# Optimization experiments

Hardware: AMD Instinct MI355X
Metric: run time of the kernel (lower is better)

The kernel has to match this reference:

```python
import jax, jax.numpy as jnp
import numpy as np

B = 2048       # batch
N = 256        # num_memory_locations
M = 64         # memory_size
U = 512        # num_units
IN = 10        # num_bits_per_vector + 2
SHIFT = 1      # conv_shift_range
CLIP = 20.0


def setup_inputs() -> dict:
    key = jax.random.key(0)
    ks = jax.random.split(key, 20)
    s = 0.05
    A0 = jax.random.uniform(ks[5], (2, B, N), dtype=jnp.float32)
    A0 = A0 / jnp.sum(A0, axis=-1, keepdims=True)  # distribution-like prev attention
    return {
        'x_t':  jax.random.normal(ks[0], (B, IN), dtype=jnp.float32),
        'H0':   jax.random.normal(ks[1], (B, U), dtype=jnp.float32) * s,
        'C0':   jax.random.normal(ks[2], (B, U), dtype=jnp.float32) * s,
        'm0':   jax.random.normal(ks[3], (B, N, M), dtype=jnp.float32) * s,
        'R0':   jax.random.normal(ks[4], (B, M), dtype=jnp.float32) * s,
        'A0':   A0,
        'Wprep': jax.random.normal(ks[6], (M, U), dtype=jnp.float32) * s,
        'bprep': jnp.zeros((U,), dtype=jnp.float32),
        'Wx':   jax.random.normal(ks[7], (IN + U, 4 * U), dtype=jnp.float32) * s,
        'Wh':   jax.random.normal(ks[8], (U, 4 * U), dtype=jnp.float32) * s,
        'bl':   jnp.zeros((4 * U,), dtype=jnp.float32),
        'Wr':   jax.random.normal(ks[9], (U, M + 6), dtype=jnp.float32) * s,
        'br':   jnp.zeros((M + 6,), dtype=jnp.float32),
        'Ww':   jax.random.normal(ks[10], (U, 3 * M + 6), dtype=jnp.float32) * s,
        'bw':   jnp.zeros((3 * M + 6,), dtype=jnp.float32),
        'Wo':   jax.random.normal(ks[11], (U + M, U), dtype=jnp.float32) * s,
        'bo':   jnp.zeros((U,), dtype=jnp.float32),
    }


def _addressing(head, m_tm1, a_tm1):
    # head: (B, >=M+6); m_tm1: (B,N,M); a_tm1: (B,N)
    k = jnp.tanh(head[:, :M])                                   # (B,M)
    beta = jax.nn.softplus(head[:, M])                          # (B,)
    g = jax.nn.sigmoid(head[:, M + 1])                          # (B,)
    s = jax.nn.softmax(head[:, M + 2:M + 2 + 2 * SHIFT + 1], axis=-1)  # (B,3)
    gamma = jax.nn.softplus(head[:, M + 2 + 2 * SHIFT + 1])     # (B,)
    # cosine similarity content addressing
    ip = jnp.einsum('bnm,bm->bn', m_tm1, k)                     # (B,N)
    k_norm = jnp.sqrt(jnp.sum(k * k, axis=1, keepdims=True))    # (B,1)
    m_norm = jnp.sqrt(jnp.sum(m_tm1 * m_tm1, axis=2))           # (B,N)
    K = ip / (k_norm * m_norm + 1e-8)
    w_c = jax.nn.softmax(beta[:, None] * K, axis=1)             # exp/sum == softmax
    w_g = g[:, None] * w_c + (1.0 - g[:, None]) * a_tm1
    # circular convolution: s placed at offsets [0..SHIFT] and [-SHIFT..-1]
    s_full = jnp.concatenate(
        [s[:, :SHIFT + 1], jnp.zeros((s.shape[0], N - (2 * SHIFT + 1)), s.dtype), s[:, -SHIFT:]],
        axis=1)                                                 # (B,N)
    idx = (jnp.arange(N)[:, None] - jnp.arange(N)[None, :]) % N  # (N,N)
    w_conv = jnp.einsum('bij,bj->bi', s_full[:, idx], w_g)       # w[i]=sum_j w_g[j]*s[(i-j)%N]
    w_sharp = w_conv ** gamma[:, None]
    return w_sharp / jnp.sum(w_sharp, axis=1, keepdims=True)


def reference(x_t, H0, C0, m0, R0, A0, Wprep, bprep, Wx, Wh, bl, Wr, br, Ww, bw, Wo, bo):
    # prep from previous reads
    h = R0 @ Wprep + bprep                                      # (B,U)
    # single-layer LSTM controller
    z = jnp.concatenate([x_t, h], axis=1) @ Wx + H0 @ Wh + bl   # (B,4U)
    i, f, g_, o = jnp.split(z, 4, axis=1)
    c_t = jax.nn.sigmoid(f) * C0 + jax.nn.sigmoid(i) * jnp.tanh(g_)
    h = jax.nn.sigmoid(o) * jnp.tanh(c_t)
    h = jnp.clip(h, -CLIP, CLIP)
    # heads
    r_out = h @ Wr + br                                         # (B, M+6)
    w_out = h @ Ww + bw                                         # (B, 3M+6)
    w_read = _addressing(r_out, m0, A0[0])                      # (B,N)
    w_write = _addressing(w_out, m0, A0[1])                     # (B,N)
    # read from OLD memory (as in original)
    R_t = jnp.einsum('bn,bnm->bm', w_read, m0)                  # (B,M)
    # write: erase + add
    del_v = jax.nn.sigmoid(w_out[:, -2 * M:-M])                 # (B,M)
    add_v = jnp.tanh(w_out[:, -M:])                             # (B,M)
    ww = w_write[:, :, None]                                    # (B,N,1)
    m_t = m0 * (1.0 - ww * del_v[:, None, :]) + ww * add_v[:, None, :]
    y_t = jnp.clip(jnp.concatenate([h, R_t], axis=1) @ Wo + bo, -CLIP, CLIP)
    return (y_t, m_t, R_t, w_read, w_write)
```

## Files before the change

### kernel.cpp

```cpp
#include <hip/hip_runtime.h>


using u16   = unsigned short;
using bfrag = __attribute__((ext_vector_type(8))) short;
using f4    = __attribute__((ext_vector_type(4))) float;

__device__ __forceinline__ float bf2f(u16 s){ union{float f;unsigned u;}v; v.u=((unsigned)s)<<16; return v.f; }
__device__ __forceinline__ u16 f2bf(float f){ union{float f;unsigned u;}v; v.f=f; unsigned r=v.u+0x7fffu+((v.u>>16)&1u); return (u16)(r>>16); }
__device__ __forceinline__ void bfpair(unsigned pr, float&a, float&b){ union{float f;unsigned u;}x,y; x.u=pr<<16; y.u=pr&0xffff0000u; a=x.f; b=y.f; }
__device__ __forceinline__ unsigned packbf(float a, float b){ return (unsigned)f2bf(a) | ((unsigned)f2bf(b)<<16); }
__device__ __forceinline__ float sigm(float x){ return 1.f/(1.f+expf(-x)); }
__device__ __forceinline__ float softplus_(float x){ return fmaxf(x,0.f)+log1pf(expf(-fabsf(x))); }

__device__ __forceinline__ void gld16(const u16* g, u16* l){
    __builtin_amdgcn_global_load_lds((const __attribute__((address_space(1))) unsigned*)g,
                                     (__attribute__((address_space(3))) unsigned*)l, 16, 0, 0);
}


__global__ __launch_bounds__(256) void k_wt_lstm(const float* __restrict__ Wx, const float* __restrict__ Wh,
                                                 u16* __restrict__ Wt){
    __shared__ float t[32][33];
    int n0 = blockIdx.x*32, k0 = blockIdx.y*32;
    int tx = threadIdx.x & 31, ty = threadIdx.x >> 5;
    #pragma unroll
    for(int r=0;r<4;r++){
        int k = k0 + ty*4 + r, n = n0 + tx;
        float v;
        if(k < 522)       v = Wx[k*2048 + n];
        else if(k < 1034) v = Wh[(k-522)*2048 + n];
        else              v = 0.f;
        t[ty*4+r][tx] = v;
    }
    __syncthreads();
    #pragma unroll
    for(int r=0;r<4;r++){
        int n = n0 + ty*4 + r, k = k0 + tx;
        Wt[n*1056 + k] = f2bf(t[tx][ty*4+r]);
    }
}

__global__ __launch_bounds__(256) void k_wt_heads(const float* __restrict__ Wr, const float* __restrict__ Ww,
                                                  u16* __restrict__ Wt){
    __shared__ float t[32][33];
    int n0 = blockIdx.x*32, k0 = blockIdx.y*32;
    int tx = threadIdx.x & 31, ty = threadIdx.x >> 5;
    #pragma unroll
    for(int r=0;r<4;r++){
        int k = k0 + ty*4 + r, n = n0 + tx;
        float v;
        if(n < 70)        v = Wr[k*70 + n];
        else if(n < 268)  v = Ww[k*198 + (n-70)];
        else              v = 0.f;
        t[ty*4+r][tx] = v;
    }
    __syncthreads();
    #pragma unroll
    for(int r=0;r<4;r++){
        int n = n0 + ty*4 + r, k = k0 + tx;
        Wt[n*512 + k] = f2bf(t[tx][ty*4+r]);
    }
}

__global__ __launch_bounds__(256) void k_wt_out(const float* __restrict__ Wo, u16* __restrict__ Wt){
    __shared__ float t[32][33];
    int n0 = blockIdx.x*32, k0 = blockIdx.y*32;
    int tx = threadIdx.x & 31, ty = threadIdx.x >> 5;
    #pragma unroll
    for(int r=0;r<4;r++){
        int k = k0 + ty*4 + r, n = n0 + tx;
        t[ty*4+r][tx] = Wo[k*512 + n];
    }
    __syncthreads();
    #pragma unroll
    for(int r=0;r<4;r++){
        int n = n0 + ty*4 + r, k = k0 + tx;
        Wt[n*576 + k] = f2bf(t[tx][ty*4+r]);
    }
}

__global__ __launch_bounds__(256) void k_abuild(const float* __restrict__ x, const float* __restrict__ H0,
                                                const float* __restrict__ R0, const float* __restrict__ Wprep,
                                                const float* __restrict__ bprep, u16* __restrict__ A){
    int flat = blockIdx.x*256 + threadIdx.x;
    int b = flat >> 9, u = flat & 511;
    u16* Ab = A + (size_t)b*1056;
    float acc = bprep[u];
    const float* r = R0 + b*64;
    #pragma unroll 8
    for(int m=0;m<64;m++) acc += r[m] * Wprep[m*512+u];
    Ab[10+u] = f2bf(acc);
    Ab[522+u] = f2bf(H0[b*512+u]);
    if(u<10) Ab[u] = f2bf(x[b*10+u]);
    if(u<22) Ab[1034+u] = 0;
}

__device__ __forceinline__ void gemm128(const u16* __restrict__ A, int lda,
                                        const u16* __restrict__ Bt, int ldb,
                                        int bm, int bn, int kiters,
                                        u16* Al, u16* Bl, f4 acc[4][4]){
    int tid = threadIdx.x, w = tid>>6, lane = tid&63, quad = lane>>4, l16 = lane&15;
    int wr = w>>1, wc = w&1;
    f4 z4 = {0.f,0.f,0.f,0.f};
    #pragma unroll
    for(int i=0;i<4;i++)
        #pragma unroll
        for(int j=0;j<4;j++) acc[i][j] = z4;
    int rA0 = tid>>2, kc = tid&3;
    int rA1 = rA0 + 64;
    const u16* ga0 = A  + (size_t)(bm+rA0)*lda + kc*8;
    const u16* ga1 = A  + (size_t)(bm+rA1)*lda + kc*8;
    const u16* gb0 = Bt + (size_t)(bn+rA0)*ldb + kc*8;
    const u16* gb1 = Bt + (size_t)(bn+rA1)*ldb + kc*8;
    u16* lA0 = Al + (w*64)*8;
    u16* lA1 = Al + (256 + w*64)*8;
    u16* lB0 = Bl + (w*64)*8;
    u16* lB1 = Bl + (256 + w*64)*8;
    for(int kt=0; kt<kiters; kt++){
        __syncthreads();
        gld16(ga0, lA0); gld16(ga1, lA1);
        gld16(gb0, lB0); gld16(gb1, lB1);
        ga0 += 32; ga1 += 32; gb0 += 32; gb1 += 32;
        __syncthreads();
        bfrag af[4], bf[4];
        #pragma unroll
        for(int i=0;i<4;i++) af[i] = *(const bfrag*)&Al[(wr*64 + i*16 + l16)*32 + quad*8];
        #pragma unroll
        for(int j=0;j<4;j++) bf[j] = *(const bfrag*)&Bl[(wc*64 + j*16 + l16)*32 + quad*8];
        #pragma unroll
        for(int i=0;i<4;i++)
            #pragma unroll
            for(int j=0;j<4;j++)
                acc[i][j] = __builtin_amdgcn_mfma_f32_16x16x32_bf16(af[i], bf[j], acc[i][j], 0, 0, 0);
    }
}

__global__ __launch_bounds__(256) void k_gemm_lstm(const u16* __restrict__ A, const u16* __restrict__ Wt,
                                                   float* __restrict__ z){
    __shared__ u16 Al[128*32], Bl[128*32];
    f4 acc[4][4];
    int bm = blockIdx.x*128, bn = blockIdx.y*128;
    gemm128(A, 1056, Wt, 1056, bm, bn, 33, Al, Bl, acc);
    int lane = threadIdx.x&63, quad = lane>>4, l16 = lane&15, w = threadIdx.x>>6;
    int wr = w>>1, wc = w&1;
    #pragma unroll
    for(int i=0;i<4;i++){
        #pragma unroll
        for(int j=0;j<4;j++){
            int col = bn + wc*64 + j*16 + l16;
            #pragma unroll
            for(int r=0;r<4;r++){
                int row = bm + wr*64 + i*16 + quad*4 + r;
                z[(size_t)row*2048 + col] = acc[i][j][r];
            }
        }
    }
}

__global__ __launch_bounds__(256) void k_gates(const float* __restrict__ z, const float* __restrict__ C0,
                                               const float* __restrict__ bl, u16* __restrict__ A2){
    int flat = blockIdx.x*256 + threadIdx.x;
    int b = flat>>9, u = flat&511;
    const float* zb = z + (size_t)b*2048;
    float zi = zb[u]      + bl[u];
    float zf = zb[512+u]  + bl[512+u];
    float zg = zb[1024+u] + bl[1024+u];
    float zo = zb[1536+u] + bl[1536+u];
    float c  = sigm(zf)*C0[b*512+u] + sigm(zi)*tanhf(zg);
    float hv = sigm(zo)*tanhf(c);
    hv = fminf(fmaxf(hv,-20.f),20.f);
    A2[(size_t)b*576 + u] = f2bf(hv);
}

__global__ __launch_bounds__(256) void k_gemm_heads(const u16* __restrict__ A2, const u16* __restrict__ Wt,
                                                    const float* __restrict__ br, const float* __restrict__ bw,
                                                    float* __restrict__ rout, float* __restrict__ wout){
    __shared__ u16 Al[128*32], Bl[128*32];
    f4 acc[4][4];
    int bm = blockIdx.x*128, bn = blockIdx.y*128;
    gemm128(A2, 576, Wt, 512, bm, bn, 16, Al, Bl, acc);
    int lane = threadIdx.x&63, quad = lane>>4, l16 = lane&15, w = threadIdx.x>>6;
    int wr = w>>1, wc = w&1;
    #pragma unroll
    for(int i=0;i<4;i++){
        #pragma unroll
        for(int j=0;j<4;j++){
            int col = bn + wc*64 + j*16 + l16;
            if(col >= 268) continue;
            #pragma unroll
            for(int r=0;r<4;r++){
                int row = bm + wr*64 + i*16 + quad*4 + r;
                float v = acc[i][j][r];
                if(col < 70) rout[(size_t)row*70 + col]        = v + br[col];
                else         wout[(size_t)row*198 + (col-70)]  = v + bw[col-70];
            }
        }
    }
}

__global__ __launch_bounds__(256) void k_gemm_out(const u16* __restrict__ A2, const u16* __restrict__ Wt,
                                                  const float* __restrict__ bo, float* __restrict__ y){
    __shared__ u16 Al[128*32], Bl[128*32];
    f4 acc[4][4];
    int bm = blockIdx.x*128, bn = blockIdx.y*128;
    gemm128(A2, 576, Wt, 576, bm, bn, 18, Al, Bl, acc);
    int lane = threadIdx.x&63, quad = lane>>4, l16 = lane&15, w = threadIdx.x>>6;
    int wr = w>>1, wc = w&1;
    #pragma unroll
    for(int i=0;i<4;i++){
        #pragma unroll
        for(int j=0;j<4;j++){
            int col = bn + wc*64 + j*16 + l16;
            float bias = bo[col];
            #pragma unroll
            for(int r=0;r<4;r++){
                int row = bm + wr*64 + i*16 + quad*4 + r;
                float v = acc[i][j][r] + bias;
                v = fminf(fmaxf(v,-20.f),20.f);
                y[(size_t)row*512 + col] = v;
            }
        }
    }
}

__global__ __launch_bounds__(256, 6) void k_addr(const float* __restrict__ m0, const float* __restrict__ A0,
                                              const float* __restrict__ rout, const float* __restrict__ wout,
                                              u16* __restrict__ A2,
                                              float* __restrict__ out_mt, float* __restrict__ out_rt,
                                              float* __restrict__ out_wr, float* __restrict__ out_ww){
    __shared__ __align__(16) float kk_s[2][64];
    __shared__ float knorm_s[2];
    __shared__ float sc[2][6];
    __shared__ float wgrr[512];
    __shared__ float wsel[2][256];
    __shared__ __align__(16) float dv[64], avv[64];
    __shared__ float wpart[4][6];
    int tid = threadIdx.x, b = blockIdx.x;
    int lane = tid & 63, w = tid >> 6;

    float a0r = A0[b*256 + tid];
    float a1r = A0[524288 + b*256 + tid];

    if(tid < 128){
        int hh = tid >> 6, m = lane;
        float kv = tanhf(hh ? wout[b*198 + m] : rout[b*70 + m]);
        kk_s[hh][m] = kv;
        float s2 = kv*kv;
        #pragma unroll
        for(int o=32;o>0;o>>=1) s2 += __shfl_xor(s2, o, 64);
        if(m == 0) knorm_s[hh] = sqrtf(s2);
    } else if(tid < 192){
        int hh = tid - 128;
        if(hh < 2){
            const float* hd = hh ? (wout + b*198) : (rout + b*70);
            sc[hh][0] = softplus_(hd[64]);
            sc[hh][1] = sigm(hd[65]);
            float e0=hd[66], e1=hd[67], e2=hd[68];
            float mx = fmaxf(e0, fmaxf(e1, e2));
            float x0=expf(e0-mx), x1=expf(e1-mx), x2=expf(e2-mx);
            float ssum = x0+x1+x2;
            sc[hh][2]=x0/ssum; sc[hh][3]=x1/ssum; sc[hh][4]=x2/ssum;
            sc[hh][5] = softplus_(hd[69]);
        }
    } else {
        int m = tid - 192;
        dv[m]  = sigm(wout[b*198 + 70 + m]);
        avv[m] = tanhf(wout[b*198 + 134 + m]);
    }
    __syncthreads();

    float ip0=0.f, ip1=0.f, ssq=0.f;
    {
        const float* mrow = m0 + (size_t)b*16384 + tid*64;
        #pragma unroll
        for(int j=0;j<16;j++){
            float4 v  = *(const float4*)(mrow + j*4);
            float4 ka = *(const float4*)&kk_s[0][j*4];
            float4 kb = *(const float4*)&kk_s[1][j*4];
            ssq += v.x*v.x + v.y*v.y + v.z*v.z + v.w*v.w;
            ip0 += v.x*ka.x + v.y*ka.y + v.z*ka.z + v.w*ka.w;
            ip1 += v.x*kb.x + v.y*kb.y + v.z*kb.z + v.w*kb.w;
        }
    }
    float mn = sqrtf(ssq);
    float K0 = ip0 / (knorm_s[0]*mn + 1e-8f);
    float K1 = ip1 / (knorm_s[1]*mn + 1e-8f);
    float e0 = sc[0][0]*K0, e1 = sc[1][0]*K1;

    float mx0 = e0, mx1 = e1;
    #pragma unroll
    for(int o=32;o>0;o>>=1){ mx0 = fmaxf(mx0, __shfl_xor(mx0,o,64)); mx1 = fmaxf(mx1, __shfl_xor(mx1,o,64)); }
    if(lane == 0){ wpart[w][0] = mx0; wpart[w][1] = mx1; }
    __syncthreads();
    mx0 = fmaxf(fmaxf(wpart[0][0],wpart[1][0]), fmaxf(wpart[2][0],wpart[3][0]));
    mx1 = fmaxf(fmaxf(wpart[0][1],wpart[1][1]), fmaxf(wpart[2][1],wpart[3][1]));
    float p0 = expf(e0-mx0), p1 = expf(e1-mx1);
    float s0 = p0, s1 = p1;
    #pragma unroll
    for(int o=32;o>0;o>>=1){ s0 += __shfl_xor(s0,o,64); s1 += __shfl_xor(s1,o,64); }
    if(lane == 0){ wpart[w][2] = s0; wpart[w][3] = s1; }
    __syncthreads();
    s0 = wpart[0][2]+wpart[1][2]+wpart[2][2]+wpart[3][2];
    s1 = wpart[0][3]+wpart[1][3]+wpart[2][3]+wpart[3][3];
    float wc0 = p0/s0, wc1 = p1/s1;

    float g0 = sc[0][1], g1 = sc[1][1];
    float wg0 = g0*wc0 + (1.f-g0)*a0r;
    float wg1 = g1*wc1 + (1.f-g1)*a1r;
    wgrr[tid] = wg0; wgrr[256+tid] = wg1;
    __syncthreads();
    int nm1 = (tid+255)&255, np1 = (tid+1)&255;
    float conv0 = sc[0][2]*wg0 + sc[0][3]*wgrr[nm1]     + sc[0][4]*wgrr[np1];
    float conv1 = sc[1][2]*wg1 + sc[1][3]*wgrr[256+nm1] + sc[1][4]*wgrr[256+np1];
    conv0 = fmaxf(conv0, 1e-35f);  conv1 = fmaxf(conv1, 1e-35f);
    float wsh0 = expf(sc[0][5]*logf(conv0));
    float wsh1 = expf(sc[1][5]*logf(conv1));
    float t0 = wsh0, t1 = wsh1;
    #pragma unroll
    for(int o=32;o>0;o>>=1){ t0 += __shfl_xor(t0,o,64); t1 += __shfl_xor(t1,o,64); }
    if(lane == 0){ wpart[w][4] = t0; wpart[w][5] = t1; }
    __syncthreads();
    t0 = wpart[0][4]+wpart[1][4]+wpart[2][4]+wpart[3][4];
    t1 = wpart[0][5]+wpart[1][5]+wpart[2][5]+wpart[3][5];
    float w0 = wsh0/t0, w1 = wsh1/t1;
    wsel[0][tid] = w0; wsel[1][tid] = w1;
    out_wr[b*256 + tid] = w0;
    out_ww[b*256 + tid] = w1;
    __syncthreads();

    float r0=0.f, r1=0.f, r2=0.f, r3=0.f;
    {
        int mc = (tid&15)*4;
        float d0=dv[mc], d1=dv[mc+1], d2=dv[mc+2], d3=dv[mc+3];
        float A0v=avv[mc], A1v=avv[mc+1], A2v=avv[mc+2], A3v=avv[mc+3];
        const float* mb = m0 + (size_t)b*16384;
        float* outb = out_mt + (size_t)b*16384;
        #pragma unroll
        for(int i=0;i<16;i++){
            int e = i*1024 + tid*4;
            int n = i*16 + (tid>>4);
            float wwv = wsel[1][n], wrv = wsel[0][n];
            float4 v = *(const float4*)(mb + e);
            float4 o;
            o.x = v.x*(1.f - wwv*d0) + wwv*A0v;
            o.y = v.y*(1.f - wwv*d1) + wwv*A1v;
            o.z = v.z*(1.f - wwv*d2) + wwv*A2v;
            o.w = v.w*(1.f - wwv*d3) + wwv*A3v;
            *(float4*)(outb + e) = o;
            r0 += wrv*v.x; r1 += wrv*v.y; r2 += wrv*v.z; r3 += wrv*v.w;
        }
    }
    {
        float* rred = wgrr;
        int g = tid>>4, mc = (tid&15)*4;
        if(g >= 8){
            rred[(g-8)*64 + mc]   = r0;
            rred[(g-8)*64 + mc+1] = r1;
            rred[(g-8)*64 + mc+2] = r2;
            rred[(g-8)*64 + mc+3] = r3;
        }
        __syncthreads();
        if(g < 8){
            rred[g*64 + mc]   += r0;
            rred[g*64 + mc+1] += r1;
            rred[g*64 + mc+2] += r2;
            rred[g*64 + mc+3] += r3;
        }
        __syncthreads();
        if(tid < 64){
            float rt = 0.f;
            #pragma unroll
            for(int g2=0; g2<8; g2++) rt += rred[g2*64 + tid];
            out_rt[b*64 + tid] = rt;
            A2[(size_t)b*576 + 512 + tid] = f2bf(rt);
        }
    }
}

extern "C" void kernel_launch(void* const* d_in, const int* in_sizes, int n_in,
                              void* d_out, int out_size, void* d_ws, size_t ws_size,
                              hipStream_t stream) {
    const float* x     = (const float*)d_in[0];
    const float* H0    = (const float*)d_in[1];
    const float* C0    = (const float*)d_in[2];
    const float* m0    = (const float*)d_in[3];
    const float* R0    = (const float*)d_in[4];
    const float* A0    = (const float*)d_in[5];
    const float* Wprep = (const float*)d_in[6];
    const float* bprep = (const float*)d_in[7];
    const float* Wx    = (const float*)d_in[8];
    const float* Wh    = (const float*)d_in[9];
    const float* bl    = (const float*)d_in[10];
    const float* Wr    = (const float*)d_in[11];
    const float* br    = (const float*)d_in[12];
    const float* Ww    = (const float*)d_in[13];
    const float* bw    = (const float*)d_in[14];
    const float* Wo    = (const float*)d_in[15];
    const float* bo    = (const float*)d_in[16];

    float* ws = (float*)d_ws;
    u16*   Wt_lstm = (u16*)(ws + 0);
    u16*   Wt_h    = (u16*)(ws + 1081344);
    u16*   Wt_o    = (u16*)(ws + 1179648);
    u16*   Abuf    = (u16*)(ws + 1327104);
    u16*   A2      = (u16*)(ws + 2408448);
    float* z       =        ws + 2998272;
    float* rout    =        ws + 7192576;
    float* wout    =        ws + 7335936;

    float* out    = (float*)d_out;
    float* out_y  = out;
    float* out_mt = out + 1048576;
    float* out_rt = out + 34603008;
    float* out_wr = out + 34734080;
    float* out_ww = out + 35258368;

    hipLaunchKernelGGL(k_wt_lstm,  dim3(64,33), dim3(256), 0, stream, Wx, Wh, Wt_lstm);
    hipLaunchKernelGGL(k_wt_heads, dim3(12,16), dim3(256), 0, stream, Wr, Ww, Wt_h);
    hipLaunchKernelGGL(k_wt_out,   dim3(16,18), dim3(256), 0, stream, Wo, Wt_o);
    hipLaunchKernelGGL(k_abuild,   dim3(4096),  dim3(256), 0, stream, x, H0, R0, Wprep, bprep, Abuf);
    hipLaunchKernelGGL(k_gemm_lstm, dim3(16,16), dim3(256), 0, stream, Abuf, Wt_lstm, z);
    hipLaunchKernelGGL(k_gates,    dim3(4096),  dim3(256), 0, stream, z, C0, bl, A2);
    hipLaunchKernelGGL(k_gemm_heads, dim3(16,3), dim3(256), 0, stream, A2, Wt_h, br, bw, rout, wout);
    hipLaunchKernelGGL(k_addr,     dim3(2048),  dim3(256), 0, stream, m0, A0, rout, wout, A2,
                       out_mt, out_rt, out_wr, out_ww);
    hipLaunchKernelGGL(k_gemm_out, dim3(16,4),  dim3(256), 0, stream, A2, Wt_o, bo, out_y);
}
```

Before: 395.9 us.

## Load memory tile once into registers and reuse for similarity and write phases

Measured after the change: 391.7 us. Within noise of the previous version (-1.0%).

```diff
diff --git a/kernel.cpp b/kernel.cpp
--- a/kernel.cpp
+++ b/kernel.cpp
@@ -223,7 +223,7 @@
     }
 }
 
-__global__ __launch_bounds__(256, 6) void k_addr(const float* __restrict__ m0, const float* __restrict__ A0,
+__global__ __launch_bounds__(256, 4) void k_addr(const float* __restrict__ m0, const float* __restrict__ A0,
                                               const float* __restrict__ rout, const float* __restrict__ wout,
                                               u16* __restrict__ A2,
                                               float* __restrict__ out_mt, float* __restrict__ out_rt,
@@ -231,15 +231,22 @@
     __shared__ __align__(16) float kk_s[2][64];
     __shared__ float knorm_s[2];
     __shared__ float sc[2][6];
+    __shared__ float ipbuf[3][256];
     __shared__ float wgrr[512];
     __shared__ float wsel[2][256];
     __shared__ __align__(16) float dv[64], avv[64];
     __shared__ float wpart[4][6];
     int tid = threadIdx.x, b = blockIdx.x;
     int lane = tid & 63, w = tid >> 6;
+    int g = tid >> 4, c = tid & 15, mc = c*4;
 
     float a0r = A0[b*256 + tid];
     float a1r = A0[524288 + b*256 + tid];
+
+    float4 v[16];
+    const float* mb = m0 + (size_t)b*16384;
+    #pragma unroll
+    for(int i=0;i<16;i++) v[i] = *(const float4*)(mb + i*1024 + tid*4);
 
     if(tid < 128){
         int hh = tid >> 6, m = lane;
@@ -269,19 +276,32 @@
     }
     __syncthreads();
 
-    float ip0=0.f, ip1=0.f, ssq=0.f;
     {
-        const float* mrow = m0 + (size_t)b*16384 + tid*64;
-        #pragma unroll
-        for(int j=0;j<16;j++){
-            float4 v  = *(const float4*)(mrow + j*4);
-            float4 ka = *(const float4*)&kk_s[0][j*4];
-            float4 kb = *(const float4*)&kk_s[1][j*4];
-            ssq += v.x*v.x + v.y*v.y + v.z*v.z + v.w*v.w;
-            ip0 += v.x*ka.x + v.y*ka.y + v.z*ka.z + v.w*ka.w;
-            ip1 += v.x*kb.x + v.y*kb.y + v.z*kb.z + v.w*kb.w;
-        }
-    }
+        float4 ka = *(const float4*)&kk_s[0][mc];
+        float4 kb = *(const float4*)&kk_s[1][mc];
+        float rip0=0.f, rip1=0.f, rssq=0.f;
+        #pragma unroll
+        for(int i=0;i<16;i++){
+            float4 t = v[i];
+            float p0 = t.x*ka.x + t.y*ka.y + t.z*ka.z + t.w*ka.w;
+            float p1 = t.x*kb.x + t.y*kb.y + t.z*kb.z + t.w*kb.w;
+            float ps = t.x*t.x + t.y*t.y + t.z*t.z + t.w*t.w;
+            #pragma unroll
+            for(int o=1;o<16;o<<=1){
+                p0 += __shfl_xor(p0, o);
+                p1 += __shfl_xor(p1, o);
+                ps += __shfl_xor(ps, o);
+            }
+            if(c == i){ rip0 = p0; rip1 = p1; rssq = ps; }
+        }
+        int idx = c*16 + g;
+        ipbuf[0][idx] = rip0;
+        ipbuf[1][idx] = rip1;
+        ipbuf[2][idx] = rssq;
+    }
+    __syncthreads();
+    float ip0 = ipbuf[0][tid], ip1 = ipbuf[1][tid], ssq = ipbuf[2][tid];
+
     float mn = sqrtf(ssq);
     float K0 = ip0 / (knorm_s[0]*mn + 1e-8f);
     float K1 = ip1 / (knorm_s[1]*mn + 1e-8f);
@@ -330,29 +350,25 @@
 
     float r0=0.f, r1=0.f, r2=0.f, r3=0.f;
     {
-        int mc = (tid&15)*4;
         float d0=dv[mc], d1=dv[mc+1], d2=dv[mc+2], d3=dv[mc+3];
         float A0v=avv[mc], A1v=avv[mc+1], A2v=avv[mc+2], A3v=avv[mc+3];
-        const float* mb = m0 + (size_t)b*16384;
         float* outb = out_mt + (size_t)b*16384;
         #pragma unroll
         for(int i=0;i<16;i++){
-            int e = i*1024 + tid*4;
-            int n = i*16 + (tid>>4);
+            int n = i*16 + g;
             float wwv = wsel[1][n], wrv = wsel[0][n];
-            float4 v = *(const float4*)(mb + e);
+            float4 t = v[i];
             float4 o;
-            o.x = v.x*(1.f - wwv*d0) + wwv*A0v;
-            o.y = v.y*(1.f - wwv*d1) + wwv*A1v;
-            o.z = v.z*(1.f - wwv*d2) + wwv*A2v;
-            o.w = v.w*(1.f - wwv*d3) + wwv*A3v;
-            *(float4*)(outb + e) = o;
-            r0 += wrv*v.x; r1 += wrv*v.y; r2 += wrv*v.z; r3 += wrv*v.w;
+            o.x = t.x*(1.f - wwv*d0) + wwv*A0v;
+            o.y = t.y*(1.f - wwv*d1) + wwv*A1v;
+            o.z = t.z*(1.f - wwv*d2) + wwv*A2v;
+            o.w = t.w*(1.f - wwv*d3) + wwv*A3v;
+            *(float4*)(outb + i*1024 + tid*4) = o;
+            r0 += wrv*t.x; r1 += wrv*t.y; r2 += wrv*t.z; r3 += wrv*t.w;
         }
     }
     {
         float* rred = wgrr;
-        int g = tid>>4, mc = (tid&15)*4;
         if(g >= 8){
             rred[(g-8)*64 + mc]   = r0;
             rred[(g-8)*64 + mc+1] = r1;
```
